# Performance work log

Hardware: AMD Instinct MI355X
Metric: run time of the kernel (lower is better)

The kernel has to match this reference:

```python
import jax, jax.numpy as jnp
import numpy as np


def setup_inputs() -> dict:
    key = jax.random.key(0)
    k1, k2, k3 = jax.random.split(key, 3)
    V, B, T = 8192, 8, 1024
    x = jax.random.randint(k1, (B, T), 0, V, dtype=jnp.int64)
    y = jax.random.randint(k2, (B, T), 0, V, dtype=jnp.int64)
    emb = jax.random.normal(k3, (V, V), dtype=jnp.float32)
    return {"x": x, "y": y, "emb": emb}


def reference(x, y, emb):
    # token embedding lookup: [B, T, C] with C == vocab_size
    logits = emb[x]
    B, T, C = logits.shape
    # Causal mean pooling. softmax over a tril(ones) mask assigns uniform
    # weight 1/(t+1) to positions 0..t, i.e. a causal running mean.
    # Equivalent to the original's avg_matrix @ logits, computed in O(T*C).
    denom = jnp.arange(1, T + 1, dtype=logits.dtype)[:, None]  # [T, 1]
    logits_prev_mean = jnp.cumsum(logits, axis=1) / denom      # [B, T, C]
    # cross_entropy with mean reduction over B*T positions
    logp = jax.nn.log_softmax(logits_prev_mean, axis=-1)
    nll = -jnp.take_along_axis(logp, y[..., None], axis=-1)[..., 0]  # [B, T]
    loss = jnp.mean(nll)
    return logits, loss
```

## Files before the change

kernel.cpp:

```cpp
#include <hip/hip_runtime.h>

#define V 8192
#define B 8
#define T 1024
#define NSEG 16
#define SEGLEN 64
#define CSLICE 1024
#define NCHUNK 32
#define CHUNK 256

__global__ __launch_bounds__(256) void gather_kernel(
    const float* __restrict__ emb, const int* __restrict__ x,
    float* __restrict__ logits, float* __restrict__ segsum)
{
    const int slice = blockIdx.x;
    const int seg   = blockIdx.y;
    const int b     = blockIdx.z;
    const int c4    = (slice * CSLICE + threadIdx.x * 4) >> 2;

    const float4* emb4    = (const float4*)emb;
    float4*       logits4 = (float4*)logits;

    float4 acc = make_float4(0.f, 0.f, 0.f, 0.f);
#pragma unroll 4
    for (int i = 0; i < SEGLEN; ++i) {
        const int t   = seg * SEGLEN + i;
        const int row = x[b * T + t];
        float4 v = emb4[(size_t)row * (V / 4) + c4];
        logits4[(size_t)(b * T + t) * (V / 4) + c4] = v;
        acc.x += v.x; acc.y += v.y; acc.z += v.z; acc.w += v.w;
    }
    ((float4*)segsum)[(size_t)(b * NSEG + seg) * (V / 4) + c4] = acc;
}

__global__ __launch_bounds__(64) void lse_kernel(
    const float* __restrict__ logits, const float* __restrict__ segsum,
    const int* __restrict__ y, float* __restrict__ P, float* __restrict__ tval)
{
    const int chunk = blockIdx.x;
    const int seg   = blockIdx.y;
    const int b     = blockIdx.z;
    const int lane  = threadIdx.x;
    const int c0    = chunk * CHUNK + lane * 4;
    const int c4    = c0 >> 2;

    const float4* ss4 = (const float4*)segsum;
    float4 S = make_float4(0.f, 0.f, 0.f, 0.f);
    for (int s = 0; s < seg; ++s) {
        float4 v = ss4[(size_t)(b * NSEG + s) * (V / 4) + c4];
        S.x += v.x; S.y += v.y; S.z += v.z; S.w += v.w;
    }

    const float4* logits4 = (const float4*)logits;
    for (int i = 0; i < SEGLEN; ++i) {
        const int t   = seg * SEGLEN + i;
        const int pos = b * T + t;
        float4 v = logits4[(size_t)pos * (V / 4) + c4];
        S.x += v.x; S.y += v.y; S.z += v.z; S.w += v.w;
        const float inv = 1.0f / (float)(t + 1);
        const float m0 = S.x * inv, m1 = S.y * inv, m2 = S.z * inv, m3 = S.w * inv;
        float e = __expf(m0) + __expf(m1) + __expf(m2) + __expf(m3);

        const int yc = y[pos];
        const unsigned d = (unsigned)(yc - c0);
        if (d < 4u) {
            const float mv = (d == 0) ? m0 : (d == 1) ? m1 : (d == 2) ? m2 : m3;
            tval[pos] = mv;
        }
#pragma unroll
        for (int off = 32; off; off >>= 1) e += __shfl_xor(e, off, 64);
        if (lane == 0) P[(size_t)chunk * (B * T) + pos] = e;
    }
}

__global__ __launch_bounds__(256) void loss_kernel(
    const float* __restrict__ P, const float* __restrict__ tval,
    float* __restrict__ loss)
{
    const int pos = blockIdx.x * 256 + threadIdx.x;
    float s = 0.f;
#pragma unroll
    for (int ch = 0; ch < NCHUNK; ++ch) s += P[(size_t)ch * (B * T) + pos];
    float nll = __logf(s) - tval[pos];

#pragma unroll
    for (int off = 32; off; off >>= 1) nll += __shfl_xor(nll, off, 64);
    __shared__ float red[4];
    const int wid = threadIdx.x >> 6;
    if ((threadIdx.x & 63) == 0) red[wid] = nll;
    __syncthreads();
    if (threadIdx.x == 0) {
        const float tot = red[0] + red[1] + red[2] + red[3];
        atomicAdd(loss, tot * (1.0f / (float)(B * T)));
    }
}

extern "C" void kernel_launch(void* const* d_in, const int* in_sizes, int n_in,
                              void* d_out, int out_size, void* d_ws, size_t ws_size,
                              hipStream_t stream) {
    const int*   x   = (const int*)d_in[0];
    const int*   y   = (const int*)d_in[1];
    const float* emb = (const float*)d_in[2];

    float* logits = (float*)d_out;
    float* loss   = logits + (size_t)B * T * V;

    float* segsum = (float*)d_ws;
    float* P      = segsum + (size_t)B * NSEG * V;
    float* tval   = P + (size_t)NCHUNK * B * T;

    gather_kernel<<<dim3(V / CSLICE, NSEG, B), 256, 0, stream>>>(emb, x, logits, segsum);
    lse_kernel<<<dim3(NCHUNK, NSEG, B), 64, 0, stream>>>(logits, segsum, y, P, tval);
    hipMemsetAsync(loss, 0, sizeof(float), stream);
    loss_kernel<<<dim3(B * T / 256), 256, 0, stream>>>(P, tval, loss);
}
```

Measured before the change: 505.3 us.

## Recompute embedding gather inside LSE kernel instead of rereading logits

The first pass now only computes per-segment column sums from the gathered embedding rows, without writing logits. The second pass re-gathers embedding rows, writes logits and computes the running-mean softmax terms in one sweep, with four waves per block. This removes the separate logits write-then-read dependency between kernels, at the cost of reading the gathered embedding rows twice. It relies on gathered rows being served partly from cache on the second read.

```diff
diff --git a/kernel.cpp b/kernel.cpp
--- a/kernel.cpp
+++ b/kernel.cpp
@@ -9,38 +9,36 @@
 #define NCHUNK 32
 #define CHUNK 256
 
-__global__ __launch_bounds__(256) void gather_kernel(
+__global__ __launch_bounds__(256) void sum_kernel(
     const float* __restrict__ emb, const int* __restrict__ x,
-    float* __restrict__ logits, float* __restrict__ segsum)
+    float* __restrict__ segsum)
 {
     const int slice = blockIdx.x;
     const int seg   = blockIdx.y;
     const int b     = blockIdx.z;
     const int c4    = (slice * CSLICE + threadIdx.x * 4) >> 2;
 
-    const float4* emb4    = (const float4*)emb;
-    float4*       logits4 = (float4*)logits;
-
+    const float4* emb4 = (const float4*)emb;
     float4 acc = make_float4(0.f, 0.f, 0.f, 0.f);
 #pragma unroll 4
     for (int i = 0; i < SEGLEN; ++i) {
-        const int t   = seg * SEGLEN + i;
-        const int row = x[b * T + t];
+        const int row = x[b * T + seg * SEGLEN + i];
         float4 v = emb4[(size_t)row * (V / 4) + c4];
-        logits4[(size_t)(b * T + t) * (V / 4) + c4] = v;
         acc.x += v.x; acc.y += v.y; acc.z += v.z; acc.w += v.w;
     }
     ((float4*)segsum)[(size_t)(b * NSEG + seg) * (V / 4) + c4] = acc;
 }
 
-__global__ __launch_bounds__(64) void lse_kernel(
-    const float* __restrict__ logits, const float* __restrict__ segsum,
-    const int* __restrict__ y, float* __restrict__ P, float* __restrict__ tval)
+__global__ __launch_bounds__(256) void fused_kernel(
+    const float* __restrict__ emb, const int* __restrict__ x,
+    const int* __restrict__ y, const float* __restrict__ segsum,
+    float* __restrict__ logits, float* __restrict__ P, float* __restrict__ tval)
 {
-    const int chunk = blockIdx.x;
+    const int wave  = threadIdx.x >> 6;
+    const int lane  = threadIdx.x & 63;
+    const int chunk = blockIdx.x * 4 + wave;
     const int seg   = blockIdx.y;
     const int b     = blockIdx.z;
-    const int lane  = threadIdx.x;
     const int c0    = chunk * CHUNK + lane * 4;
     const int c4    = c0 >> 2;
 
@@ -51,11 +49,14 @@
         S.x += v.x; S.y += v.y; S.z += v.z; S.w += v.w;
     }
 
-    const float4* logits4 = (const float4*)logits;
+    const float4* emb4    = (const float4*)emb;
+    float4*       logits4 = (float4*)logits;
     for (int i = 0; i < SEGLEN; ++i) {
         const int t   = seg * SEGLEN + i;
         const int pos = b * T + t;
-        float4 v = logits4[(size_t)pos * (V / 4) + c4];
+        const int row = x[pos];
+        float4 v = emb4[(size_t)row * (V / 4) + c4];
+        logits4[(size_t)pos * (V / 4) + c4] = v;
         S.x += v.x; S.y += v.y; S.z += v.z; S.w += v.w;
         const float inv = 1.0f / (float)(t + 1);
         const float m0 = S.x * inv, m1 = S.y * inv, m2 = S.z * inv, m3 = S.w * inv;
@@ -109,8 +110,8 @@
     float* P      = segsum + (size_t)B * NSEG * V;
     float* tval   = P + (size_t)NCHUNK * B * T;
 
-    gather_kernel<<<dim3(V / CSLICE, NSEG, B), 256, 0, stream>>>(emb, x, logits, segsum);
-    lse_kernel<<<dim3(NCHUNK, NSEG, B), 64, 0, stream>>>(logits, segsum, y, P, tval);
     hipMemsetAsync(loss, 0, sizeof(float), stream);
+    sum_kernel<<<dim3(V / CSLICE, NSEG, B), 256, 0, stream>>>(emb, x, segsum);
+    fused_kernel<<<dim3(NCHUNK / 4, NSEG, B), 256, 0, stream>>>(emb, x, y, segsum, logits, P, tval);
     loss_kernel<<<dim3(B * T / 256), 256, 0, stream>>>(P, tval, loss);
 }
```

Result: faster. 484.9 us (-4.0%).
